# Performance work log

Measured on AMD Instinct MI355X. Metric: run time of the kernel, lower is better.

The kernel has to match this reference:

```python
import jax, jax.numpy as jnp
import numpy as np

EPS = 1e-7  # keras.backend.epsilon()
ROUTINGS = 3
NUM_CAPSULE = 32
DIM_CAPSULE = 64


def squash(x, axis=-1):
    # NOTE: faithful to the repo's (non-standard) squash: x / sqrt(||x||^2 + eps)
    s = jnp.sum(jnp.square(x), axis=axis, keepdims=True)
    return x / jnp.sqrt(s + EPS)


def setup_inputs() -> dict:
    key = jax.random.key(0)
    k1, k2 = jax.random.split(key)
    B, N_in, D_in = 64, 1024, 512
    u_vecs = jax.random.normal(k1, (B, N_in, D_in), dtype=jnp.float32)
    # shared capsule kernel: (1, input_dim, num_capsule * dim_capsule)
    W = jax.random.normal(k2, (1, D_in, NUM_CAPSULE * DIM_CAPSULE), dtype=jnp.float32) * (1.0 / np.sqrt(D_in))
    return {"u_vecs": u_vecs, "W": W}


def reference(u_vecs, W):
    B, N_in, D_in = u_vecs.shape
    # K.conv1d with a width-1 kernel == pointwise matmul
    u_hat = jnp.einsum('bid,dz->biz', u_vecs, W[0])  # [B, N_in, NC*DC]
    u_hat = u_hat.reshape(B, N_in, NUM_CAPSULE, DIM_CAPSULE)
    u_hat = jnp.transpose(u_hat, (0, 2, 1, 3))  # [B, NC, N_in, DC]

    b = jnp.zeros((B, NUM_CAPSULE, N_in), dtype=u_hat.dtype)
    outputs = None
    for i in range(ROUTINGS):
        # original permutes b to [B, N_in, NC] and softmaxes the last axis,
        # i.e. softmax over the output-capsule axis (axis=1 here)
        c = jax.nn.softmax(b, axis=1)  # [B, NC, N_in]
        outputs = squash(jnp.einsum('bni,bnid->bnd', c, u_hat))  # [B, NC, DC]
        if i < ROUTINGS - 1:
            b = jnp.einsum('bnd,bnid->bni', outputs, u_hat)  # agreement logits
    return outputs
```

## Files before the change

### kernel.cpp

```cpp
#include <hip/hip_runtime.h>

#define B_SZ   64
#define N_IN   1024
#define D_IN   512
#define NC     32
#define DC     64

typedef unsigned short u16;
typedef __bf16 bf16x8 __attribute__((ext_vector_type(8)));
typedef unsigned short u16x8 __attribute__((ext_vector_type(8)));
typedef float f32x4  __attribute__((ext_vector_type(4)));
typedef float f32x16 __attribute__((ext_vector_type(16)));

__device__ __forceinline__ float bf2f(u16 u) {
    unsigned x = ((unsigned)u) << 16;
    return __builtin_bit_cast(float, x);
}
__device__ __forceinline__ u16 f2bf(float f) {
    unsigned x = __builtin_bit_cast(unsigned, f);
    unsigned r = (x + 0x7fffu + ((x >> 16) & 1u)) >> 16;
    return (u16)r;
}

#define ASYNC_LDS16(g, l) __builtin_amdgcn_global_load_lds( \
    (const __attribute__((address_space(1))) void*)(g),     \
    (__attribute__((address_space(3))) void*)(l), 16, 0, 0)

__global__ __launch_bounds__(256) void conv_rowsum(const float* __restrict__ A,
                                                   u16* __restrict__ Ab,
                                                   float* __restrict__ Arow) {
    const int tid = threadIdx.x;
    const int b  = blockIdx.x >> 3;
    const int r0 = (blockIdx.x & 7) << 7;
    const size_t base = ((size_t)(b * N_IN + r0)) * 512 + tid * 2;
    const float* p = A + base;
    u16* q = Ab + base;
    float a0 = 0.f, a1 = 0.f;
    for (int r = 0; r < 128; ++r) {
        float2 v = *(const float2*)(p + (size_t)r * 512);
        a0 += v.x; a1 += v.y;
        unsigned pk = (unsigned)f2bf(v.x) | ((unsigned)f2bf(v.y) << 16);
        *(unsigned*)(q + (size_t)r * 512) = pk;
    }
    atomicAdd(&Arow[b * 512 + tid * 2], a0);
    atomicAdd(&Arow[b * 512 + tid * 2 + 1], a1);
}

__global__ __launch_bounds__(256) void s0_squash(const float* __restrict__ Arow,
                                                 const float* __restrict__ W,
                                                 float* __restrict__ outs) {
    const int tid = threadIdx.x;
    const int z   = blockIdx.x * 256 + tid;
    const int bg  = blockIdx.y * 4;
    float acc[4] = {};
    for (int k = 0; k < 512; ++k) {
        float wv = W[(size_t)k * 2048 + z];
#pragma unroll
        for (int bb = 0; bb < 4; ++bb)
            acc[bb] += Arow[(bg + bb) * 512 + k] * wv;
    }
#pragma unroll
    for (int bb = 0; bb < 4; ++bb) {
        float v = acc[bb] * 0.03125f;
        float sq = v * v;
        for (int off = 32; off; off >>= 1) sq += __shfl_xor(sq, off);
        outs[(size_t)(bg + bb) * 2048 + z] = v * (1.0f / sqrtf(sq + 1e-7f));
    }
}

__global__ __launch_bounds__(256) void g_pack(const float* __restrict__ W,
                                              const float* __restrict__ outs,
                                              u16* __restrict__ Gpack) {
    __shared__ float vl[64 * 130];
    const int tid = threadIdx.x;
    const int kt  = blockIdx.x;
    const int np  = blockIdx.y;

    for (int t = tid; t < 8192; t += 256) {
        int b = t >> 7, idx = t & 127;
        vl[b * 130 + idx] = outs[(size_t)b * 2048 + np * 128 + idx];
    }
    __syncthreads();

    const int bs = tid & 15;
    const int k  = kt * 16 + (tid >> 4);
    float acc[4][2] = {};
    for (int n2 = 0; n2 < 2; ++n2) {
        const float* wr = W + (size_t)k * 2048 + (np * 2 + n2) * 64;
        for (int d = 0; d < 64; ++d) {
            float wv = wr[d];
#pragma unroll
            for (int bb = 0; bb < 4; ++bb)
                acc[bb][n2] += wv * vl[(bs + 16 * bb) * 130 + n2 * 64 + d];
        }
    }
    const int kk = k >> 5, kq = k & 31;
#pragma unroll
    for (int bb = 0; bb < 4; ++bb)
#pragma unroll
        for (int n2 = 0; n2 < 2; ++n2) {
            int b = bs + 16 * bb, n = np * 2 + n2;
            Gpack[(((size_t)b * 16 + kk) * 32 + n) * 32 + kq] = f2bf(acc[bb][n2]);
        }
}

__global__ __launch_bounds__(256, 2) void routing_mfma(const u16* __restrict__ Ab,
                                                       const u16* __restrict__ Gpack,
                                                       float* __restrict__ Mp) {
    __shared__ u16   Al[64 * 512];
    __shared__ float cl[64 * 33];
    const int tid   = threadIdx.x;
    const int lane  = tid & 63;
    const int w     = __builtin_amdgcn_readfirstlane(tid >> 6);
    const int b     = blockIdx.x >> 4;
    const int chunk = blockIdx.x & 15;
    const int row0  = chunk * 64;

    const size_t rowbase = (size_t)(b * N_IN + row0);
#pragma unroll
    for (int rr = 0; rr < 16; ++rr) {
        const int r   = w * 16 + rr;
        const int sig = (lane & 56) | ((lane & 7) ^ (r & 7));
        ASYNC_LDS16(Ab + (rowbase + r) * 512 + sig * 8, &Al[r * 512]);
    }
    __syncthreads();

    const int quad = lane >> 4;
    const int l16  = lane & 15;
    f32x4 lacc[2] = {};
    const u16* gb = Gpack + (size_t)b * 16384;
    {
        const int r  = w * 16 + l16;
        const u16* ar = &Al[r * 512];
        for (int kk = 0; kk < 16; ++kk) {
            const int c  = kk * 4 + quad;
            const int cs = (c & 56) | ((c & 7) ^ (r & 7));
            bf16x8 af = *(const bf16x8*)&ar[cs * 8];
#pragma unroll
            for (int nt = 0; nt < 2; ++nt) {
                bf16x8 bf = *(const bf16x8*)&gb[(kk * 32 + nt * 16 + l16) * 32 + quad * 8];
                lacc[nt] = __builtin_amdgcn_mfma_f32_16x16x32_bf16(af, bf, lacc[nt], 0, 0, 0);
            }
        }
    }
#pragma unroll
    for (int nt = 0; nt < 2; ++nt)
#pragma unroll
        for (int reg = 0; reg < 4; ++reg)
            cl[(w * 16 + quad * 4 + reg) * 33 + nt * 16 + l16] = lacc[nt][reg];
    __syncthreads();

    if (tid < 64) {
        float* row = &cl[tid * 33];
        float mx = row[0];
        for (int k = 1; k < NC; ++k) mx = fmaxf(mx, row[k]);
        float ssum = 0.f;
        for (int k = 0; k < NC; ++k) { float t = __expf(row[k] - mx); row[k] = t; ssum += t; }
        float inv = 1.f / ssum;
        for (int k = 0; k < NC; ++k) row[k] *= inv;
    }
    __syncthreads();

    const int h   = lane >> 5;
    const int l32 = lane & 31;
    bf16x8 cfrag[4];
#pragma unroll
    for (int kk2 = 0; kk2 < 4; ++kk2) {
        u16x8 t;
#pragma unroll
        for (int j = 0; j < 8; ++j)
            t[j] = f2bf(cl[(kk2 * 16 + h * 8 + j) * 33 + l32]);
        cfrag[kk2] = __builtin_bit_cast(bf16x8, t);
    }
    float* mpb = Mp + ((size_t)b * 16 + chunk) * 32 * 512;
    for (int cti = 0; cti < 4; ++cti) {
        const int ct   = w * 4 + cti;
        const int kcol = ct * 32 + l32;
        const int c2   = kcol >> 3;
        const int e    = kcol & 7;
        f32x16 acc = {};
#pragma unroll
        for (int kk2 = 0; kk2 < 4; ++kk2) {
            u16x8 t;
#pragma unroll
            for (int j = 0; j < 8; ++j) {
                const int r2  = kk2 * 16 + h * 8 + j;
                const int cs2 = (c2 & 56) | ((c2 & 7) ^ (r2 & 7));
                t[j] = Al[r2 * 512 + cs2 * 8 + e];
            }
            bf16x8 bf = __builtin_bit_cast(bf16x8, t);
            acc = __builtin_amdgcn_mfma_f32_32x32x16_bf16(cfrag[kk2], bf, acc, 0, 0, 0);
        }
#pragma unroll
        for (int reg = 0; reg < 16; ++reg) {
            const int n = (reg & 3) + 8 * (reg >> 2) + 4 * h;
            mpb[(size_t)n * 512 + kcol] = acc[reg];
        }
    }
}

__global__ __launch_bounds__(256, 2) void s_final(const float* __restrict__ Mp,
                                                  const float* __restrict__ W,
                                                  float* __restrict__ outs,
                                                  float* __restrict__ outf) {
    __shared__ u16   Wl[512 * 64];
    __shared__ float Ml[8 * 512];
    const int tid = threadIdx.x;
    const int n   = blockIdx.x;
    const int bg  = blockIdx.y * 8;

    for (int t = tid; t < 32768; t += 256) {
        int k = t >> 6, d = t & 63;
        Wl[t] = f2bf(W[(size_t)k * 2048 + n * 64 + d]);
    }
    for (int t = tid; t < 4096; t += 256) {
        int bs = t >> 9, k = t & 511;
        const float* p = Mp + (((size_t)(bg + bs) * 16) * 32 + n) * 512 + k;
        float s = 0.f;
#pragma unroll
        for (int ch = 0; ch < 16; ++ch) s += p[(size_t)ch * 32 * 512];
        Ml[t] = s;
    }
    __syncthreads();

    const int w = tid >> 6;
    const int d = tid & 63;
    float acc[2] = {};
    for (int k = 0; k < 512; ++k) {
        float wv = bf2f(Wl[k * 64 + d]);
        acc[0] += Ml[(w * 2) * 512 + k] * wv;
        acc[1] += Ml[(w * 2 + 1) * 512 + k] * wv;
    }
#pragma unroll
    for (int i = 0; i < 2; ++i) {
        const int b = bg + w * 2 + i;
        float sq = acc[i] * acc[i];
        for (int off = 32; off; off >>= 1) sq += __shfl_xor(sq, off);
        float o = acc[i] * (1.0f / sqrtf(sq + 1e-7f));
        size_t idx = (size_t)b * 2048 + n * 64 + d;
        outs[idx] = o;
        if (outf) outf[idx] = o;
    }
}

extern "C" void kernel_launch(void* const* d_in, const int* in_sizes, int n_in,
                              void* d_out, int out_size, void* d_ws, size_t ws_size,
                              hipStream_t stream) {
    (void)in_sizes; (void)n_in; (void)out_size; (void)ws_size;
    const float* A = (const float*)d_in[0];
    const float* W = (const float*)d_in[1];
    float* out     = (float*)d_out;

    uint8_t* ws = (uint8_t*)d_ws;
    const size_t AB_B    = (size_t)B_SZ * N_IN * D_IN * 2;
    const size_t AROW_B  = (size_t)B_SZ * D_IN * 4;
    const size_t OUTS_B  = (size_t)B_SZ * NC * DC * 4;
    const size_t GP_B    = (size_t)B_SZ * 16 * 32 * 32 * 2;
    u16*   Ab    = (u16*)ws;
    float* Arow  = (float*)(ws + AB_B);
    float* outs  = (float*)(ws + AB_B + AROW_B);
    u16*   Gpack = (u16*)(ws + AB_B + AROW_B + OUTS_B);
    float* Mp    = (float*)(ws + AB_B + AROW_B + OUTS_B + GP_B);

    hipMemsetAsync(Arow, 0, AROW_B, stream);
    conv_rowsum<<<512, 256, 0, stream>>>(A, Ab, Arow);
    s0_squash<<<dim3(8, 16), 256, 0, stream>>>(Arow, W, outs);

    for (int it = 0; it < 2; ++it) {
        g_pack<<<dim3(32, 16), 256, 0, stream>>>(W, outs, Gpack);
        routing_mfma<<<1024, 256, 0, stream>>>(Ab, Gpack, Mp);
        s_final<<<dim3(32, 8), 256, 0, stream>>>(Mp, W, outs, it == 1 ? out : nullptr);
    }
}
```

Measured before the change: 401.0 us.

## Shrink intermediates to half precision, pre-convert W, register-level softmax

Several changes are made at once. W is converted to bf16 once up front and read in that form by g_pack and s_final. The per-chunk partial sums Mp are stored as fp16 instead of fp32, halving that write and read traffic. The routing softmax now runs in registers with wave shuffles instead of one serial thread per row in shared memory. conv_rowsum is widened to float4 loads. The aim is less memory traffic and less serialization, at the cost of extra rounding from fp16 storage of the partial sums and bf16 W in g_pack.

```diff
diff --git a/kernel.cpp b/kernel.cpp
--- a/kernel.cpp
+++ b/kernel.cpp
@@ -7,6 +7,7 @@
 #define DC     64
 
 typedef unsigned short u16;
+typedef unsigned int   u32;
 typedef __bf16 bf16x8 __attribute__((ext_vector_type(8)));
 typedef unsigned short u16x8 __attribute__((ext_vector_type(8)));
 typedef float f32x4  __attribute__((ext_vector_type(4)));
@@ -21,10 +22,26 @@
     unsigned r = (x + 0x7fffu + ((x >> 16) & 1u)) >> 16;
     return (u16)r;
 }
+__device__ __forceinline__ u16 f2h(float f) {
+    return __builtin_bit_cast(u16, (_Float16)f);
+}
+__device__ __forceinline__ float h2f(u16 h) {
+    return (float)__builtin_bit_cast(_Float16, h);
+}
 
 #define ASYNC_LDS16(g, l) __builtin_amdgcn_global_load_lds( \
     (const __attribute__((address_space(1))) void*)(g),     \
     (__attribute__((address_space(3))) void*)(l), 16, 0, 0)
+
+__global__ __launch_bounds__(256) void w_conv(const float* __restrict__ W,
+                                              u16* __restrict__ Wb) {
+    const int i = blockIdx.x * 256 + threadIdx.x;
+    float4 v = ((const float4*)W)[i];
+    uint2 pk;
+    pk.x = (u32)f2bf(v.x) | ((u32)f2bf(v.y) << 16);
+    pk.y = (u32)f2bf(v.z) | ((u32)f2bf(v.w) << 16);
+    ((uint2*)Wb)[i] = pk;
+}
 
 __global__ __launch_bounds__(256) void conv_rowsum(const float* __restrict__ A,
                                                    u16* __restrict__ Ab,
@@ -32,18 +49,23 @@
     const int tid = threadIdx.x;
     const int b  = blockIdx.x >> 3;
     const int r0 = (blockIdx.x & 7) << 7;
-    const size_t base = ((size_t)(b * N_IN + r0)) * 512 + tid * 2;
-    const float* p = A + base;
-    u16* q = Ab + base;
-    float a0 = 0.f, a1 = 0.f;
-    for (int r = 0; r < 128; ++r) {
-        float2 v = *(const float2*)(p + (size_t)r * 512);
-        a0 += v.x; a1 += v.y;
-        unsigned pk = (unsigned)f2bf(v.x) | ((unsigned)f2bf(v.y) << 16);
-        *(unsigned*)(q + (size_t)r * 512) = pk;
-    }
-    atomicAdd(&Arow[b * 512 + tid * 2], a0);
-    atomicAdd(&Arow[b * 512 + tid * 2 + 1], a1);
+    const int q  = tid & 127;
+    const int rh = tid >> 7;
+    const size_t rowbase = (size_t)(b * N_IN + r0);
+    float a0 = 0.f, a1 = 0.f, a2 = 0.f, a3 = 0.f;
+    for (int r = rh; r < 128; r += 2) {
+        float4 v = *(const float4*)(A + (rowbase + r) * 512 + q * 4);
+        a0 += v.x; a1 += v.y; a2 += v.z; a3 += v.w;
+        uint2 pk;
+        pk.x = (u32)f2bf(v.x) | ((u32)f2bf(v.y) << 16);
+        pk.y = (u32)f2bf(v.z) | ((u32)f2bf(v.w) << 16);
+        *(uint2*)(Ab + (rowbase + r) * 512 + q * 4) = pk;
+    }
+    float* ar = Arow + b * 512 + q * 4;
+    atomicAdd(ar + 0, a0);
+    atomicAdd(ar + 1, a1);
+    atomicAdd(ar + 2, a2);
+    atomicAdd(ar + 3, a3);
 }
 
 __global__ __launch_bounds__(256) void s0_squash(const float* __restrict__ Arow,
@@ -68,7 +90,7 @@
     }
 }
 
-__global__ __launch_bounds__(256) void g_pack(const float* __restrict__ W,
+__global__ __launch_bounds__(256) void g_pack(const u16* __restrict__ Wb,
                                               const float* __restrict__ outs,
                                               u16* __restrict__ Gpack) {
     __shared__ float vl[64 * 130];
@@ -86,9 +108,9 @@
     const int k  = kt * 16 + (tid >> 4);
     float acc[4][2] = {};
     for (int n2 = 0; n2 < 2; ++n2) {
-        const float* wr = W + (size_t)k * 2048 + (np * 2 + n2) * 64;
+        const u16* wr = Wb + (size_t)k * 2048 + (np * 2 + n2) * 64;
         for (int d = 0; d < 64; ++d) {
-            float wv = wr[d];
+            float wv = bf2f(wr[d]);
 #pragma unroll
             for (int bb = 0; bb < 4; ++bb)
                 acc[bb][n2] += wv * vl[(bs + 16 * bb) * 130 + n2 * 64 + d];
@@ -106,9 +128,9 @@
 
 __global__ __launch_bounds__(256, 2) void routing_mfma(const u16* __restrict__ Ab,
                                                        const u16* __restrict__ Gpack,
-                                                       float* __restrict__ Mp) {
-    __shared__ u16   Al[64 * 512];
-    __shared__ float cl[64 * 33];
+                                                       u16* __restrict__ Mp) {
+    __shared__ u16 Al[64 * 512];
+    __shared__ u16 clb[64 * 34];
     const int tid   = threadIdx.x;
     const int lane  = tid & 63;
     const int w     = __builtin_amdgcn_readfirstlane(tid >> 6);
@@ -143,21 +165,25 @@
             }
         }
     }
-#pragma unroll
-    for (int nt = 0; nt < 2; ++nt)
-#pragma unroll
-        for (int reg = 0; reg < 4; ++reg)
-            cl[(w * 16 + quad * 4 + reg) * 33 + nt * 16 + l16] = lacc[nt][reg];
-    __syncthreads();
-
-    if (tid < 64) {
-        float* row = &cl[tid * 33];
-        float mx = row[0];
-        for (int k = 1; k < NC; ++k) mx = fmaxf(mx, row[k]);
-        float ssum = 0.f;
-        for (int k = 0; k < NC; ++k) { float t = __expf(row[k] - mx); row[k] = t; ssum += t; }
-        float inv = 1.f / ssum;
-        for (int k = 0; k < NC; ++k) row[k] *= inv;
+
+#pragma unroll
+    for (int reg = 0; reg < 4; ++reg) {
+        float m = fmaxf(lacc[0][reg], lacc[1][reg]);
+        m = fmaxf(m, __shfl_xor(m, 1));
+        m = fmaxf(m, __shfl_xor(m, 2));
+        m = fmaxf(m, __shfl_xor(m, 4));
+        m = fmaxf(m, __shfl_xor(m, 8));
+        float e0 = __expf(lacc[0][reg] - m);
+        float e1 = __expf(lacc[1][reg] - m);
+        float s = e0 + e1;
+        s += __shfl_xor(s, 1);
+        s += __shfl_xor(s, 2);
+        s += __shfl_xor(s, 4);
+        s += __shfl_xor(s, 8);
+        float inv = 1.f / s;
+        const int row = w * 16 + quad * 4 + reg;
+        clb[row * 34 + l16]      = f2bf(e0 * inv);
+        clb[row * 34 + 16 + l16] = f2bf(e1 * inv);
     }
     __syncthreads();
 
@@ -169,10 +195,10 @@
         u16x8 t;
 #pragma unroll
         for (int j = 0; j < 8; ++j)
-            t[j] = f2bf(cl[(kk2 * 16 + h * 8 + j) * 33 + l32]);
+            t[j] = clb[(kk2 * 16 + h * 8 + j) * 34 + l32];
         cfrag[kk2] = __builtin_bit_cast(bf16x8, t);
     }
-    float* mpb = Mp + ((size_t)b * 16 + chunk) * 32 * 512;
+    u16* mpb = Mp + ((size_t)b * 16 + chunk) * 32 * 512;
     for (int cti = 0; cti < 4; ++cti) {
         const int ct   = w * 4 + cti;
         const int kcol = ct * 32 + l32;
@@ -194,13 +220,13 @@
 #pragma unroll
         for (int reg = 0; reg < 16; ++reg) {
             const int n = (reg & 3) + 8 * (reg >> 2) + 4 * h;
-            mpb[(size_t)n * 512 + kcol] = acc[reg];
-        }
-    }
-}
-
-__global__ __launch_bounds__(256, 2) void s_final(const float* __restrict__ Mp,
-                                                  const float* __restrict__ W,
+            mpb[(size_t)n * 512 + kcol] = f2h(acc[reg]);
+        }
+    }
+}
+
+__global__ __launch_bounds__(256, 2) void s_final(const u16* __restrict__ Mp,
+                                                  const u16* __restrict__ Wb,
                                                   float* __restrict__ outs,
                                                   float* __restrict__ outf) {
     __shared__ u16   Wl[512 * 64];
@@ -209,17 +235,22 @@
     const int n   = blockIdx.x;
     const int bg  = blockIdx.y * 8;
 
-    for (int t = tid; t < 32768; t += 256) {
-        int k = t >> 6, d = t & 63;
-        Wl[t] = f2bf(W[(size_t)k * 2048 + n * 64 + d]);
-    }
-    for (int t = tid; t < 4096; t += 256) {
-        int bs = t >> 9, k = t & 511;
-        const float* p = Mp + (((size_t)(bg + bs) * 16) * 32 + n) * 512 + k;
-        float s = 0.f;
-#pragma unroll
-        for (int ch = 0; ch < 16; ++ch) s += p[(size_t)ch * 32 * 512];
-        Ml[t] = s;
+    for (int t = tid; t < 8192; t += 256) {
+        int k = t >> 4, d4 = t & 15;
+        ((uint2*)Wl)[t] = *(const uint2*)(Wb + (size_t)k * 2048 + n * 64 + d4 * 4);
+    }
+    for (int t = tid; t < 2048; t += 256) {
+        int bs = t >> 8, kp = t & 255;
+        const u32* p = (const u32*)(Mp + (((size_t)(bg + bs) * 16) * 32 + n) * 512) + kp;
+        float s0 = 0.f, s1 = 0.f;
+#pragma unroll
+        for (int ch = 0; ch < 16; ++ch) {
+            u32 v = p[(size_t)ch * 32 * 256];
+            s0 += h2f((u16)(v & 0xffffu));
+            s1 += h2f((u16)(v >> 16));
+        }
+        Ml[bs * 512 + kp * 2]     = s0;
+        Ml[bs * 512 + kp * 2 + 1] = s1;
     }
     __syncthreads();
 
@@ -256,19 +287,23 @@
     const size_t AROW_B  = (size_t)B_SZ * D_IN * 4;
     const size_t OUTS_B  = (size_t)B_SZ * NC * DC * 4;
     const size_t GP_B    = (size_t)B_SZ * 16 * 32 * 32 * 2;
+    const size_t WB_B    = (size_t)D_IN * NC * DC * 2;
     u16*   Ab    = (u16*)ws;
     float* Arow  = (float*)(ws + AB_B);
     float* outs  = (float*)(ws + AB_B + AROW_B);
     u16*   Gpack = (u16*)(ws + AB_B + AROW_B + OUTS_B);
-    float* Mp    = (float*)(ws + AB_B + AROW_B + OUTS_B + GP_B);
-
+    u16*   Wb    = (u16*)(ws + AB_B + AROW_B + OUTS_B + GP_B);
+    u16*   Mp    = (u16*)(ws + AB_B + AROW_B + OUTS_B + GP_B + WB_B);
+
+    w_conv<<<1024, 256, 0, stream>>>(W, Wb);
     hipMemsetAsync(Arow, 0, AROW_B, stream);
     conv_rowsum<<<512, 256, 0, stream>>>(A, Ab, Arow);
+
     s0_squash<<<dim3(8, 16), 256, 0, stream>>>(Arow, W, outs);
 
     for (int it = 0; it < 2; ++it) {
-        g_pack<<<dim3(32, 16), 256, 0, stream>>>(W, outs, Gpack);
+        g_pack<<<dim3(32, 16), 256, 0, stream>>>(Wb, outs, Gpack);
         routing_mfma<<<1024, 256, 0, stream>>>(Ab, Gpack, Mp);
-        s_final<<<dim3(32, 8), 256, 0, stream>>>(Mp, W, outs, it == 1 ? out : nullptr);
-    }
-}
+        s_final<<<dim3(32, 8), 256, 0, stream>>>(Mp, Wb, outs, it == 1 ? out : nullptr);
+    }
+}
```

After: 383.9 us. 1.04x faster.
